# Kernel optimization log

Measured on AMD Instinct MI355X. Metric: run time of the kernel, lower is better.

Reference implementation:

```python
import jax, jax.numpy as jnp
import numpy as np

EMBED_DIM = 1024


def setup_inputs() -> dict:
    key = jax.random.key(0)
    ks = jax.random.split(key, 8)
    B, S, D = 4, 2048, EMBED_DIM
    scale = 1.0 / np.sqrt(D)
    x = jax.random.normal(ks[0], (B, S, D), dtype=jnp.float32)
    mask = jnp.zeros((S, S), dtype=jnp.float32)
    # nn.Linear default init ~ U(-1/sqrt(fan_in), 1/sqrt(fan_in)); exact dist irrelevant for correctness
    w_q = jax.random.uniform(ks[1], (D, D), jnp.float32, -scale, scale)
    b_q = jax.random.uniform(ks[2], (D,), jnp.float32, -scale, scale)
    w_k = jax.random.uniform(ks[3], (D, D), jnp.float32, -scale, scale)
    b_k = jax.random.uniform(ks[4], (D,), jnp.float32, -scale, scale)
    w_v = jax.random.uniform(ks[5], (D, D), jnp.float32, -scale, scale)
    b_v = jax.random.uniform(ks[6], (D,), jnp.float32, -scale, scale)
    return {"x": x, "mask": mask, "w_q": w_q, "b_q": b_q,
            "w_k": w_k, "b_k": b_k, "w_v": w_v, "b_v": b_v}


def reference(x, mask, w_q, b_q, w_k, b_k, w_v, b_v):
    D = x.shape[-1]
    # nn.Linear computes x @ W^T + b
    Q = jnp.einsum('bsd,ed->bse', x, w_q) + b_q
    K = jnp.einsum('bsd,ed->bse', x, w_k) + b_k
    V = jnp.einsum('bsd,ed->bse', x, w_v) + b_v
    scores = jnp.einsum('bqd,bkd->bqk', Q, K) / jnp.sqrt(jnp.asarray(D, x.dtype))
    scores = scores + mask  # additive mask, broadcast over batch
    attn = jax.nn.softmax(scores, axis=-1)
    return jnp.einsum('bqk,bkd->bqd', attn, V)
```

## Files before the change

kernel.cpp:

```cpp
#include <hip/hip_runtime.h>


typedef __attribute__((ext_vector_type(8))) short short8;
typedef __attribute__((ext_vector_type(4))) short short4v;
typedef __attribute__((ext_vector_type(4))) float float4v;

__device__ __forceinline__ short f2bf(float f) {
  unsigned u = __builtin_bit_cast(unsigned, f);
  u += 0x7fffu + ((u >> 16) & 1u);
  return (short)(u >> 16);
}
__device__ __forceinline__ float bf2f(short s) {
  unsigned u = ((unsigned)(unsigned short)s) << 16;
  return __builtin_bit_cast(float, u);
}

__device__ __forceinline__ void gl2lds16(const void* g, void* l) {
  __builtin_amdgcn_global_load_lds((const __attribute__((address_space(1))) void*)g,
                                   (__attribute__((address_space(3))) void*)l, 16, 0, 0);
}

__global__ __launch_bounds__(256) void prep_kernel(const float* __restrict__ x,
                                                   const float* __restrict__ wq,
                                                   const float* __restrict__ wk,
                                                   const float* __restrict__ wv,
                                                   const float* __restrict__ bq,
                                                   const float* __restrict__ bk,
                                                   short* __restrict__ x_bf,
                                                   short* __restrict__ w_bf,
                                                   float* __restrict__ bcat) {
  int b = blockIdx.x;
  if (b < 3072) {
    int seg = b >> 10;
    const float* w = seg == 0 ? wq : (seg == 1 ? wk : wv);
    int i = (b - (seg << 10)) * 256 + threadIdx.x;
    float4v v = ((const float4v*)w)[i];
    short4v o;
    o.x = f2bf(v.x); o.y = f2bf(v.y); o.z = f2bf(v.z); o.w = f2bf(v.w);
    ((short4v*)(w_bf + (long)seg * 1048576))[i] = o;
  } else if (b < 11264) {
    int i = (b - 3072) * 256 + threadIdx.x;
    float4v v = ((const float4v*)x)[i];
    short4v o;
    o.x = f2bf(v.x); o.y = f2bf(v.y); o.z = f2bf(v.z); o.w = f2bf(v.w);
    ((short4v*)x_bf)[i] = o;
  } else {
    int i = (b - 11264) * 256 + threadIdx.x;
    if (i < 2048) bcat[i] = i < 1024 ? bq[i] : bk[i - 1024];
  }
}

__global__ __launch_bounds__(256) void zero_rs(float* __restrict__ rs) {
  rs[blockIdx.x * 256 + threadIdx.x] = 0.f;
}

template <int EPI, int BM>
__device__ __forceinline__ void gemm_body(const short* __restrict__ A,
                                          const short* __restrict__ Bm,
                                          void* __restrict__ C,
                                          const float* __restrict__ aux,
                                          float* __restrict__ rsum, float scale,
                                          int N, int Kd, int Bld, int m0, int n0,
                                          short (*As)[64], short (*Bs)[64]) {
  constexpr int WI = BM / 32;
  const int t = threadIdx.x;
  const int lane = t & 63, wave = t >> 6;
  const int wm = (wave & 1) * (BM / 2), wn = (wave >> 1) * 64;
  const int col = lane & 15, quad = lane >> 4;

  const int r_loc = lane >> 3, slot = lane & 7;
  const int cch = slot ^ r_loc;
  const int sw = col & 7;

  float4v acc[WI][4] = {};

  for (int kt = 0; kt < Kd; kt += 64) {
#pragma unroll
    for (int u = 0; u < WI; ++u) {
      const int rowbase = wave * (BM / 4) + u * 8;
      gl2lds16(&A[(long)(m0 + rowbase + r_loc) * Kd + kt + cch * 8],
               &As[rowbase][0] + lane * 8);
    }
#pragma unroll
    for (int u = 0; u < 4; ++u) {
      const int rowbase = wave * 32 + u * 8;
      gl2lds16(&Bm[(long)(n0 + rowbase + r_loc) * Bld + kt + cch * 8],
               &Bs[rowbase][0] + lane * 8);
    }
    __syncthreads();

#pragma unroll
    for (int s = 0; s < 2; ++s) {
      short8 af[WI], bfr[4];
#pragma unroll
      for (int i = 0; i < WI; ++i)
        af[i] = *(const short8*)&As[wm + i * 16 + col][((s * 4 + quad) ^ sw) * 8];
#pragma unroll
      for (int j = 0; j < 4; ++j)
        bfr[j] = *(const short8*)&Bs[wn + j * 16 + col][((s * 4 + quad) ^ sw) * 8];
#pragma unroll
      for (int i = 0; i < WI; ++i)
#pragma unroll
        for (int j = 0; j < 4; ++j)
          acc[i][j] = __builtin_amdgcn_mfma_f32_16x16x32_bf16(af[i], bfr[j], acc[i][j], 0, 0, 0);
    }
    __syncthreads();
  }

  const float LOG2E = 1.44269504f;
  const float c1 = scale * LOG2E;
#pragma unroll
  for (int i = 0; i < WI; ++i) {
    float invv[4], addm[4], rsum4[4] = {0.f, 0.f, 0.f, 0.f};
    if (EPI == 2) {
#pragma unroll
      for (int r = 0; r < 4; ++r)
        invv[r] = __builtin_amdgcn_rcpf(aux[m0 + wm + i * 16 + quad * 4 + r]);
    }
    if (EPI == 3) {
#pragma unroll
      for (int r = 0; r < 4; ++r) addm[r] = aux[m0 + wm + i * 16 + quad * 4 + r];
    }
#pragma unroll
    for (int j = 0; j < 4; ++j) {
      const int n = n0 + wn + j * 16 + col;
      float addn = 0.f;
      if (EPI == 0) addn = aux[n];
#pragma unroll
      for (int r = 0; r < 4; ++r) {
        const int m = m0 + wm + i * 16 + quad * 4 + r;
        float v = acc[i][j][r];
        if (EPI == 0) {
          ((short*)C)[(long)m * N + n] = f2bf(v + addn);
        } else if (EPI == 1) {
          float mv = aux[(long)m * N + n];
          float e = exp2f(fmaf(v, c1, mv * LOG2E));
          short q = f2bf(e);
          ((short*)C)[(long)m * N + n] = q;
          rsum4[r] += bf2f(q);
        } else if (EPI == 2) {
          ((float*)C)[(long)m * N + n] = v * invv[r];
        } else {
          ((short*)C)[(long)m * N + n] = f2bf(v + addm[r]);
        }
      }
    }
    if (EPI == 1) {
#pragma unroll
      for (int r = 0; r < 4; ++r) {
        float s = rsum4[r];
        s += __shfl_xor(s, 1);
        s += __shfl_xor(s, 2);
        s += __shfl_xor(s, 4);
        s += __shfl_xor(s, 8);
        if (col == 0) atomicAdd(&rsum[m0 + wm + i * 16 + quad * 4 + r], s);
      }
    }
  }
}

__global__ __launch_bounds__(256) void qkv_kernel(const short* __restrict__ x_bf,
                                                  const short* __restrict__ w_bf,
                                                  short* __restrict__ QK,
                                                  short* __restrict__ Vt,
                                                  const float* __restrict__ bcat,
                                                  const float* __restrict__ bv) {
  __shared__ alignas(16) short As[128][64];
  __shared__ alignas(16) short Bs[128][64];
  const int b = blockIdx.x;
  if (b < 1024) {
    const int bz = b >> 9, r = b & 511;
    gemm_body<0, 128>(x_bf, w_bf + (long)bz * 1048576, QK + (long)bz * 8388608,
                      bcat + bz * 1024, nullptr, 1.f,
                      1024, 1024, 1024, (r & 63) * 128, (r >> 6) * 128, As, Bs);
  } else {
    const int r = b - 1024;
    gemm_body<3, 128>(w_bf + 2097152, x_bf, Vt, bv, nullptr, 1.f,
                      8192, 1024, 1024, (r & 7) * 128, (r >> 3) * 128, As, Bs);
  }
}

__global__ __launch_bounds__(256) void scores_kernel(const short* __restrict__ Q,
                                                     const short* __restrict__ Kb,
                                                     short* __restrict__ P,
                                                     const float* __restrict__ mask,
                                                     float* __restrict__ rs) {
  __shared__ alignas(16) short As[128][64];
  __shared__ alignas(16) short Bs[128][64];
  const int bz = blockIdx.z;
  gemm_body<1, 128>(Q + (long)bz * 2097152, Kb + (long)bz * 2097152,
                    P + (long)bz * 4194304, mask, rs + bz * 2048, 0.03125f,
                    2048, 1024, 1024, blockIdx.x * 128, blockIdx.y * 128, As, Bs);
}

__global__ __launch_bounds__(256) void pv_kernel(const short* __restrict__ P,
                                                 const short* __restrict__ Vt,
                                                 float* __restrict__ out,
                                                 const float* __restrict__ rs) {
  __shared__ alignas(16) short As[64][64];
  __shared__ alignas(16) short Bs[128][64];
  const int bz = blockIdx.z;
  gemm_body<2, 64>(P + (long)bz * 4194304, Vt + (long)bz * 2048,
                   out + (long)bz * 2097152, rs + bz * 2048, nullptr, 1.f,
                   1024, 2048, 8192, blockIdx.x * 64, blockIdx.y * 128, As, Bs);
}

extern "C" void kernel_launch(void* const* d_in, const int* in_sizes, int n_in,
                              void* d_out, int out_size, void* d_ws, size_t ws_size,
                              hipStream_t stream) {
  const float* x    = (const float*)d_in[0];
  const float* mask = (const float*)d_in[1];
  const float* wq   = (const float*)d_in[2];
  const float* bq   = (const float*)d_in[3];
  const float* wk   = (const float*)d_in[4];
  const float* bk   = (const float*)d_in[5];
  const float* wv   = (const float*)d_in[6];
  const float* bv   = (const float*)d_in[7];
  float* out = (float*)d_out;

  char* ws = (char*)d_ws;
  const size_t MB = 1024 * 1024;
  short* x_bf = (short*)(ws);
  short* w_bf = (short*)(ws + 16 * MB);
  float* rs   = (float*)(ws + 16 * MB);
  short* QK   = (short*)(ws + 22 * MB);
  short* Vt   = (short*)(ws + 54 * MB);
  short* P    = (short*)(ws + 70 * MB);
  float* bcat = (float*)(ws + 70 * MB);

  prep_kernel<<<11272, 256, 0, stream>>>(x, wq, wk, wv, bq, bk, x_bf, w_bf, bcat);

  qkv_kernel<<<1536, 256, 0, stream>>>(x_bf, w_bf, QK, Vt, bcat, bv);

  zero_rs<<<32, 256, 0, stream>>>(rs);

  short* Q  = QK;
  short* Kb = QK + 8388608;

  scores_kernel<<<dim3(16, 16, 4), 256, 0, stream>>>(Q, Kb, P, mask, rs);

  pv_kernel<<<dim3(32, 8, 4), 256, 0, stream>>>(P, Vt, out, rs);
}
```

Measured before the change: 283.1 us.

## Replace row-sum atomics with partial buffers, remap block order, enlarge PV tile

Row sums are no longer accumulated with atomics into a zeroed buffer. Each scores block writes partial sums into a per-column-tile slot, and the PV kernel reduces the 32 partials into shared memory before scaling. This removes the zero_rs launch. All GEMM grids become 1D with a remapped block order, presumably to group blocks that share tiles for cache reuse across XCDs. The PV kernel moves to 128x128 tiles, which halves its block count and adds a small reduction step in the epilogue.

Result: faster. 273.0 us (-3.6%).

```diff
diff --git a/kernel.cpp b/kernel.cpp
--- a/kernel.cpp
+++ b/kernel.cpp
@@ -50,11 +50,7 @@
   }
 }
 
-__global__ __launch_bounds__(256) void zero_rs(float* __restrict__ rs) {
-  rs[blockIdx.x * 256 + threadIdx.x] = 0.f;
-}
-
-template <int EPI, int BM>
+template <int EPI>
 __device__ __forceinline__ void gemm_body(const short* __restrict__ A,
                                           const short* __restrict__ Bm,
                                           void* __restrict__ C,
@@ -62,28 +58,23 @@
                                           float* __restrict__ rsum, float scale,
                                           int N, int Kd, int Bld, int m0, int n0,
                                           short (*As)[64], short (*Bs)[64]) {
-  constexpr int WI = BM / 32;
   const int t = threadIdx.x;
   const int lane = t & 63, wave = t >> 6;
-  const int wm = (wave & 1) * (BM / 2), wn = (wave >> 1) * 64;
+  const int wm = (wave & 1) * 64, wn = (wave >> 1) * 64;
   const int col = lane & 15, quad = lane >> 4;
 
   const int r_loc = lane >> 3, slot = lane & 7;
   const int cch = slot ^ r_loc;
   const int sw = col & 7;
 
-  float4v acc[WI][4] = {};
+  float4v acc[4][4] = {};
 
   for (int kt = 0; kt < Kd; kt += 64) {
 #pragma unroll
-    for (int u = 0; u < WI; ++u) {
-      const int rowbase = wave * (BM / 4) + u * 8;
+    for (int u = 0; u < 4; ++u) {
+      const int rowbase = wave * 32 + u * 8;
       gl2lds16(&A[(long)(m0 + rowbase + r_loc) * Kd + kt + cch * 8],
                &As[rowbase][0] + lane * 8);
-    }
-#pragma unroll
-    for (int u = 0; u < 4; ++u) {
-      const int rowbase = wave * 32 + u * 8;
       gl2lds16(&Bm[(long)(n0 + rowbase + r_loc) * Bld + kt + cch * 8],
                &Bs[rowbase][0] + lane * 8);
     }
@@ -91,15 +82,15 @@
 
 #pragma unroll
     for (int s = 0; s < 2; ++s) {
-      short8 af[WI], bfr[4];
-#pragma unroll
-      for (int i = 0; i < WI; ++i)
+      short8 af[4], bfr[4];
+#pragma unroll
+      for (int i = 0; i < 4; ++i)
         af[i] = *(const short8*)&As[wm + i * 16 + col][((s * 4 + quad) ^ sw) * 8];
 #pragma unroll
       for (int j = 0; j < 4; ++j)
         bfr[j] = *(const short8*)&Bs[wn + j * 16 + col][((s * 4 + quad) ^ sw) * 8];
 #pragma unroll
-      for (int i = 0; i < WI; ++i)
+      for (int i = 0; i < 4; ++i)
 #pragma unroll
         for (int j = 0; j < 4; ++j)
           acc[i][j] = __builtin_amdgcn_mfma_f32_16x16x32_bf16(af[i], bfr[j], acc[i][j], 0, 0, 0);
@@ -107,15 +98,25 @@
     __syncthreads();
   }
 
+  float* invb = (float*)Bs;
+  if (EPI == 2) {
+    if (t < 128) {
+      float s = 0.f;
+#pragma unroll
+      for (int p = 0; p < 32; ++p) s += aux[p * 8192 + m0 + t];
+      invb[t] = __builtin_amdgcn_rcpf(s);
+    }
+    __syncthreads();
+  }
+
   const float LOG2E = 1.44269504f;
   const float c1 = scale * LOG2E;
 #pragma unroll
-  for (int i = 0; i < WI; ++i) {
+  for (int i = 0; i < 4; ++i) {
     float invv[4], addm[4], rsum4[4] = {0.f, 0.f, 0.f, 0.f};
     if (EPI == 2) {
 #pragma unroll
-      for (int r = 0; r < 4; ++r)
-        invv[r] = __builtin_amdgcn_rcpf(aux[m0 + wm + i * 16 + quad * 4 + r]);
+      for (int r = 0; r < 4; ++r) invv[r] = invb[wm + i * 16 + quad * 4 + r];
     }
     if (EPI == 3) {
 #pragma unroll
@@ -153,7 +154,8 @@
         s += __shfl_xor(s, 2);
         s += __shfl_xor(s, 4);
         s += __shfl_xor(s, 8);
-        if (col == 0) atomicAdd(&rsum[m0 + wm + i * 16 + quad * 4 + r], s);
+        if (col == 0)
+          rsum[(wn >> 6) * 8192 + m0 + wm + i * 16 + quad * 4 + r] = s;
       }
     }
   }
@@ -169,14 +171,17 @@
   __shared__ alignas(16) short Bs[128][64];
   const int b = blockIdx.x;
   if (b < 1024) {
-    const int bz = b >> 9, r = b & 511;
-    gemm_body<0, 128>(x_bf, w_bf + (long)bz * 1048576, QK + (long)bz * 8388608,
-                      bcat + bz * 1024, nullptr, 1.f,
-                      1024, 1024, 1024, (r & 63) * 128, (r >> 6) * 128, As, Bs);
+    const int g = (b & 7) * 128 + (b >> 3);
+    const int bz = g >> 9, rr = g & 511;
+    const int m0 = (rr >> 3) * 128, n0 = (rr & 7) * 128;
+    gemm_body<0>(x_bf, w_bf + (long)bz * 1048576, QK + (long)bz * 8388608,
+                 bcat + bz * 1024, nullptr, 1.f, 1024, 1024, 1024, m0, n0, As, Bs);
   } else {
-    const int r = b - 1024;
-    gemm_body<3, 128>(w_bf + 2097152, x_bf, Vt, bv, nullptr, 1.f,
-                      8192, 1024, 1024, (r & 7) * 128, (r >> 3) * 128, As, Bs);
+    const int v = b - 1024;
+    const int g = (v & 7) * 64 + (v >> 3);
+    const int m0 = (g >> 6) * 128, n0 = (g & 63) * 128;
+    gemm_body<3>(w_bf + 2097152, x_bf, Vt, bv, nullptr, 1.f,
+                 8192, 1024, 1024, m0, n0, As, Bs);
   }
 }
 
@@ -184,25 +189,32 @@
                                                      const short* __restrict__ Kb,
                                                      short* __restrict__ P,
                                                      const float* __restrict__ mask,
-                                                     float* __restrict__ rs) {
+                                                     float* __restrict__ rspart) {
   __shared__ alignas(16) short As[128][64];
   __shared__ alignas(16) short Bs[128][64];
-  const int bz = blockIdx.z;
-  gemm_body<1, 128>(Q + (long)bz * 2097152, Kb + (long)bz * 2097152,
-                    P + (long)bz * 4194304, mask, rs + bz * 2048, 0.03125f,
-                    2048, 1024, 1024, blockIdx.x * 128, blockIdx.y * 128, As, Bs);
+  const int id = blockIdx.x;
+  const int g = (id & 7) * 128 + (id >> 3);
+  const int bz = g >> 8, t2 = g & 255;
+  const int m0 = (t2 >> 4) * 128, n0 = (t2 & 15) * 128;
+  gemm_body<1>(Q + (long)bz * 2097152, Kb + (long)bz * 2097152,
+               P + (long)bz * 4194304, mask,
+               rspart + (n0 >> 7) * 2 * 8192 + bz * 2048, 0.03125f,
+               2048, 1024, 1024, m0, n0, As, Bs);
 }
 
 __global__ __launch_bounds__(256) void pv_kernel(const short* __restrict__ P,
                                                  const short* __restrict__ Vt,
                                                  float* __restrict__ out,
-                                                 const float* __restrict__ rs) {
-  __shared__ alignas(16) short As[64][64];
+                                                 const float* __restrict__ rspart) {
+  __shared__ alignas(16) short As[128][64];
   __shared__ alignas(16) short Bs[128][64];
-  const int bz = blockIdx.z;
-  gemm_body<2, 64>(P + (long)bz * 4194304, Vt + (long)bz * 2048,
-                   out + (long)bz * 2097152, rs + bz * 2048, nullptr, 1.f,
-                   1024, 2048, 8192, blockIdx.x * 64, blockIdx.y * 128, As, Bs);
+  const int id = blockIdx.x;
+  const int g = (id & 7) * 64 + (id >> 3);
+  const int bz = g >> 7, t2 = g & 127;
+  const int m0 = (t2 >> 3) * 128, n0 = (t2 & 7) * 128;
+  gemm_body<2>(P + (long)bz * 4194304, Vt + (long)bz * 2048,
+               out + (long)bz * 2097152, rspart + bz * 2048, nullptr, 1.f,
+               1024, 2048, 8192, m0, n0, As, Bs);
 }
 
 extern "C" void kernel_launch(void* const* d_in, const int* in_sizes, int n_in,
@@ -220,24 +232,22 @@
 
   char* ws = (char*)d_ws;
   const size_t MB = 1024 * 1024;
-  short* x_bf = (short*)(ws);
-  short* w_bf = (short*)(ws + 16 * MB);
-  float* rs   = (float*)(ws + 16 * MB);
-  short* QK   = (short*)(ws + 22 * MB);
-  short* Vt   = (short*)(ws + 54 * MB);
-  short* P    = (short*)(ws + 70 * MB);
-  float* bcat = (float*)(ws + 70 * MB);
+  short* x_bf   = (short*)(ws);
+  float* rspart = (float*)(ws);
+  short* w_bf   = (short*)(ws + 16 * MB);
+  short* QK     = (short*)(ws + 22 * MB);
+  short* Vt     = (short*)(ws + 54 * MB);
+  short* P      = (short*)(ws + 70 * MB);
+  float* bcat   = (float*)(ws + 70 * MB);
 
   prep_kernel<<<11272, 256, 0, stream>>>(x, wq, wk, wv, bq, bk, x_bf, w_bf, bcat);
 
   qkv_kernel<<<1536, 256, 0, stream>>>(x_bf, w_bf, QK, Vt, bcat, bv);
-
-  zero_rs<<<32, 256, 0, stream>>>(rs);
 
   short* Q  = QK;
   short* Kb = QK + 8388608;
 
-  scores_kernel<<<dim3(16, 16, 4), 256, 0, stream>>>(Q, Kb, P, mask, rs);
-
-  pv_kernel<<<dim3(32, 8, 4), 256, 0, stream>>>(P, Vt, out, rs);
-}
+  scores_kernel<<<1024, 256, 0, stream>>>(Q, Kb, P, mask, rspart);
+
+  pv_kernel<<<512, 256, 0, stream>>>(P, Vt, out, rspart);
+}
```
